# Kernel tuning notes

Hardware: AMD Instinct MI355X
Metric: run time of the kernel (lower is better)

The kernel has to match this reference:

```python
import jax, jax.numpy as jnp
import numpy as np
import itertools


def _dwconv(x, w, b, pad, dil):
    # depthwise conv3d, x: [B,C,H,W,D], w: [C,1,k,k,k]
    out = jax.lax.conv_general_dilated(
        x, w, (1, 1, 1), [(pad, pad)] * 3, rhs_dilation=(dil, dil, dil),
        dimension_numbers=('NCDHW', 'OIDHW', 'NCDHW'), feature_group_count=x.shape[1])
    return out + b[None, :, None, None, None]


def _conv(x, w, b, pad):
    out = jax.lax.conv_general_dilated(
        x, w, (1, 1, 1), [(pad, pad)] * 3,
        dimension_numbers=('NCDHW', 'OIDHW', 'NCDHW'))
    return out + b[None, :, None, None, None]


def _pw(x, w, b):
    # 1x1x1 conv: x [B,C,H,W,D], w [O,C]
    return jnp.einsum('bchwd,oc->bohwd', x, w) + b[None, :, None, None, None]


def _deform_conv3d(x, off_w, off_b, w, b):
    # DeformConvPack-style: offsets from a regular 3x3x3 conv, then
    # trilinearly-interpolated gather at (base + kernel tap + offset), then GEMM.
    B, C, H, W, D = x.shape
    K = 27
    dt = x.dtype
    off = _conv(x, off_w, off_b, 1).reshape(B, K, 3, H, W, D)  # per-tap (dh,dw,dd)
    gh = jnp.arange(H, dtype=dt)
    gw = jnp.arange(W, dtype=dt)
    gd = jnp.arange(D, dtype=dt)
    base = jnp.stack(jnp.meshgrid(gh, gw, gd, indexing='ij'), 0)  # [3,H,W,D]
    t = jnp.arange(-1, 2, dtype=dt)  # kernel taps, padding=1
    taps = jnp.stack(jnp.meshgrid(t, t, t, indexing='ij'), -1).reshape(K, 3)
    pos = base[None] + taps[:, :, None, None, None]  # [K,3,H,W,D]
    pos = pos[None] + off  # [B,K,3,H,W,D]
    i0 = jnp.floor(pos)
    frac = pos - i0  # [B,K,3,H,W,D]
    i0 = i0.astype(jnp.int32)
    N = H * W * D
    xf = x.reshape(B, C, N)
    hi = jnp.array([H - 1, W - 1, D - 1], jnp.int32)[None, None, :, None, None, None]
    acc = jnp.zeros((B, C, K * N), dt)
    for corner in itertools.product((0, 1), repeat=3):
        c = jnp.array(corner, jnp.int32)[None, None, :, None, None, None]
        idx = i0 + c
        wgt = jnp.prod(jnp.where(c == 1, frac, 1.0 - frac), axis=2)  # [B,K,H,W,D]
        valid = jnp.all((idx >= 0) & (idx <= hi), axis=2)
        ic = jnp.clip(idx, 0, hi)
        flat = (ic[:, :, 0] * W + ic[:, :, 1]) * D + ic[:, :, 2]  # [B,K,H,W,D]
        g = jnp.take_along_axis(xf, flat.reshape(B, 1, K * N), axis=2)  # [B,C,K*N]
        acc = acc + g * (wgt * valid.astype(dt)).reshape(B, 1, K * N)
    sampled = acc.reshape(B, C, K, N)
    out = jnp.einsum('bckn,ock->bon', sampled, w.reshape(w.shape[0], C, K))
    out = out + b[None, :, None]
    return out.reshape(B, -1, H, W, D)


def _forward(x, proj1_w, proj1_b, conv0_w, conv0_b, convsp_w, convsp_b,
             off_w, off_b, dcn_w, dcn_b, conv1_w, conv1_b, proj2_w, proj2_b,
             B, C, H, W, D):
    xv = jnp.transpose(x, (0, 2, 1)).reshape(B, C, H, W, D)
    shortcut = xv
    h = jax.nn.gelu(_pw(xv, proj1_w, proj1_b), approximate=False)
    u = h
    a = _dwconv(h, conv0_w, conv0_b, 2, 1)        # 5x5x5 depthwise
    a = _dwconv(a, convsp_w, convsp_b, 9, 3)      # 7x7x7 depthwise, dilation 3
    a = _deform_conv3d(a, off_w, off_b, dcn_w, dcn_b)
    a = _pw(a, conv1_w, conv1_b)
    h = u * a
    h = _pw(h, proj2_w, proj2_b)
    out = h + shortcut
    return jnp.transpose(out.reshape(B, C, H * W * D), (0, 2, 1))


def setup_inputs() -> dict:
    key = jax.random.key(0)
    ks = jax.random.split(key, 8)
    B, C, H, W, D = 1, 64, 32, 32, 32
    N = H * W * D
    r = lambda k, s, sc: jax.random.normal(k, s, jnp.float32) * np.float32(sc)
    inv = lambda f: 1.0 / np.sqrt(f)
    return {
        'x': jax.random.normal(ks[0], (B, N, C), jnp.float32),
        'proj1_w': r(ks[1], (C, C), inv(C)), 'proj1_b': jnp.zeros((C,), jnp.float32),
        'conv0_w': r(ks[2], (C, 1, 5, 5, 5), inv(125)), 'conv0_b': jnp.zeros((C,), jnp.float32),
        'convsp_w': r(ks[3], (C, 1, 7, 7, 7), inv(343)), 'convsp_b': jnp.zeros((C,), jnp.float32),
        'off_w': r(ks[4], (81, C, 3, 3, 3), 0.01 * inv(27 * C)), 'off_b': jnp.zeros((81,), jnp.float32),
        'dcn_w': r(ks[5], (C, C, 3, 3, 3), inv(27 * C)), 'dcn_b': jnp.zeros((C,), jnp.float32),
        'conv1_w': r(ks[6], (C, C), inv(C)), 'conv1_b': jnp.zeros((C,), jnp.float32),
        'proj2_w': r(ks[7], (C, C), inv(C)), 'proj2_b': jnp.zeros((C,), jnp.float32),
        'B': B, 'C': C, 'H': H, 'W': W, 'D': D,
    }


def reference(x, proj1_w, proj1_b, conv0_w, conv0_b, convsp_w, convsp_b,
              off_w, off_b, dcn_w, dcn_b, conv1_w, conv1_b, proj2_w, proj2_b,
              B, C, H, W, D):
    return _forward(x, proj1_w, proj1_b, conv0_w, conv0_b, convsp_w, convsp_b,
                    off_w, off_b, dcn_w, dcn_b, conv1_w, conv1_b, proj2_w, proj2_b,
                    B, C, H, W, D)
```

## Files before the change

kernel.cpp:

```cpp
#include <hip/hip_runtime.h>
#include <math.h>

#define NSP 32768
#define NCH 64

typedef _Float16 half8 __attribute__((ext_vector_type(8)));
typedef _Float16 half4 __attribute__((ext_vector_type(4)));
typedef _Float16 half2v __attribute__((ext_vector_type(2)));
typedef float f32x4 __attribute__((ext_vector_type(4)));

__global__ __launch_bounds__(256) void k_proj1m(const float* __restrict__ x,
        const half8* __restrict__ Wp1, const float* __restrict__ b,
        _Float16* __restrict__ Uh) {
    __shared__ __align__(16) _Float16 Sx[64 * 72];
    int t = threadIdx.x;
    int n0 = blockIdx.x * 64;
    int lane = t & 63, wv = t >> 6;
    for (int i = wv; i < 64; i += 4) {
        float v = x[(size_t)(n0 + i) * 64 + lane];
        Sx[i * 72 + lane] = (_Float16)v;
    }
    __syncthreads();
    int pl = lane & 15, g = lane >> 4;
    int ob = wv;
    const half8* wbase = Wp1 + ob * 64 + lane;
    #pragma unroll
    for (int nt = 0; nt < 4; ++nt) {
        f32x4 acc4 = {0.f, 0.f, 0.f, 0.f};
        const _Float16* sb = &Sx[(nt * 16 + pl) * 72 + g * 8];
        #pragma unroll
        for (int kb = 0; kb < 2; ++kb) {
            half8 af = wbase[kb * 256];
            half8 bf = *(const half8*)(sb + kb * 32);
            acc4 = __builtin_amdgcn_mfma_f32_16x16x32_f16(af, bf, acc4, 0, 0, 0);
        }
        int n = n0 + nt * 16 + pl;
        #pragma unroll
        for (int r = 0; r < 4; ++r) {
            int o = ob * 16 + g * 4 + r;
            float a = acc4[r] + b[o];
            float gv = 0.5f * a * (1.0f + erff(a * 0.70710678118654752f));
            Uh[(size_t)o * NSP + n] = (_Float16)gv;
        }
    }
}

__global__ __launch_bounds__(256) void k_dw5(const _Float16* __restrict__ in,
        const float* __restrict__ w, const float* __restrict__ b,
        _Float16* __restrict__ out) {
    __shared__ float Sb5[2][20 * 38];
    int t = threadIdx.x;
    int bid = blockIdx.x;
    int blk = (bid & 7) * 128 + (bid >> 3);
    int c  = blk >> 4;
    int hq = (blk >> 1) & 7;
    int wq = blk & 1;
    int d  = t & 31;
    int wbloc = t >> 5;
    int wb = wq * 8 + wbloc;
    const float* wc = w + c * 125;
    const _Float16* src = in + ((size_t)c << 15);

    for (int idx = t; idx < 160; idx += 256) {
        int bi = idx / 80, r = idx % 80;
        int wi = r >> 2, e = r & 3;
        int Dp = (e < 2) ? e : 32 + e;
        Sb5[bi][wi * 38 + Dp] = 0.f;
    }

    float bc = b[c];
    float acc[4][2];
    #pragma unroll
    for (int a = 0; a < 4; ++a) { acc[a][0] = bc; acc[a][1] = bc; }

    #define STAGE5(m)                                                        \
        { int hh_ = 4 * hq + (m) - 2;                                        \
          if ((unsigned)hh_ < 32u) {                                         \
            const _Float16* row_ = src + (hh_ << 10);                        \
            for (int idx = t; idx < 80; idx += 256) {                        \
                int wi = idx >> 2, oct = idx & 3;                            \
                int wj = 16 * wq - 2 + wi;                                   \
                half8 vv = (half8)(_Float16)0.f;                             \
                if ((unsigned)wj < 32u)                                      \
                    vv = *(const half8*)&row_[(wj << 5) + oct * 8];          \
                float* dst = &Sb5[(m) & 1][wi * 38 + 2 + oct * 8];           \
                dst[0] = (float)vv[0]; dst[1] = (float)vv[1];                \
                dst[2] = (float)vv[2]; dst[3] = (float)vv[3];                \
                dst[4] = (float)vv[4]; dst[5] = (float)vv[5];                \
                dst[6] = (float)vv[6]; dst[7] = (float)vv[7];                \
            } } }

    STAGE5(0)
    __syncthreads();
    #pragma unroll 1
    for (int m = 0; m < 8; ++m) {
        if (m < 7) STAGE5(m + 1)
        int hh = 4 * hq + m - 2;
        if ((unsigned)hh < 32u) {
            float v[6][5];
            const float* sb = &Sb5[m & 1][0];
            #pragma unroll
            for (int jc = 0; jc < 6; ++jc)
                #pragma unroll
                for (int l = 0; l < 5; ++l)
                    v[jc][l] = sb[(2 * wbloc + jc) * 38 + d + l];
            #pragma unroll
            for (int a = 0; a < 4; ++a) {
                if (a <= m && m <= a + 4) {
                    const float* wr = wc + (m - a) * 25;
                    float s0 = 0.f, s1 = 0.f;
                    #pragma unroll
                    for (int j = 0; j < 5; ++j)
                        #pragma unroll
                        for (int l = 0; l < 5; ++l) {
                            float wv2 = wr[j * 5 + l];
                            s0 += wv2 * v[j][l];
                            s1 += wv2 * v[j + 1][l];
                        }
                    acc[a][0] += s0;
                    acc[a][1] += s1;
                }
            }
        }
        __syncthreads();
    }
    #pragma unroll
    for (int a = 0; a < 4; ++a)
        #pragma unroll
        for (int bb = 0; bb < 2; ++bb)
            out[(size_t)c * NSP + ((4 * hq + a) << 10) + ((2 * wb + bb) << 5) + d]
                = (_Float16)acc[a][bb];
    #undef STAGE5
}

__global__ __launch_bounds__(256) void k_dw7(const _Float16* __restrict__ in,
        const float* __restrict__ w, const float* __restrict__ b,
        _Float16* __restrict__ out) {
    __shared__ float Sb7[2][26 * 52];
    int t = threadIdx.x;
    int bid = blockIdx.x;
    int blk = (bid & 7) * 96 + (bid >> 3);
    int c  = blk / 12;
    int h0 = (blk % 12) >> 2;
    int wq = blk & 3;
    int d  = t & 31;
    int wloc = t >> 5;
    int w_ = wq * 8 + wloc;
    const float* wc = w + c * 343;
    const _Float16* src = in + ((size_t)c << 15);

    for (int idx = t; idx < 936; idx += 256) {
        int bi = idx / 468, r = idx % 468;
        int wi = r / 18, e = r % 18;
        int Dp = (e < 9) ? e : 32 + e;
        Sb7[bi][wi * 52 + Dp] = 0.f;
    }

    float bc = b[c];
    float acc[11];
    #pragma unroll
    for (int a = 0; a < 11; ++a) acc[a] = bc;

    #define STAGE7(m)                                                        \
        { int hh_ = h0 + 3 * (m) - 9;                                        \
          if ((unsigned)hh_ < 32u) {                                         \
            const _Float16* row_ = src + (hh_ << 10);                        \
            for (int idx = t; idx < 104; idx += 256) {                       \
                int wi = idx >> 2, oct = idx & 3;                            \
                int wj = 8 * wq - 9 + wi;                                    \
                half8 vv = (half8)(_Float16)0.f;                             \
                if ((unsigned)wj < 32u)                                      \
                    vv = *(const half8*)&row_[(wj << 5) + oct * 8];          \
                float* dst = &Sb7[(m) & 1][wi * 52 + 9 + oct * 8];           \
                dst[0] = (float)vv[0]; dst[1] = (float)vv[1];                \
                dst[2] = (float)vv[2]; dst[3] = (float)vv[3];                \
                dst[4] = (float)vv[4]; dst[5] = (float)vv[5];                \
                dst[6] = (float)vv[6]; dst[7] = (float)vv[7];                \
            } } }

    STAGE7(0)
    __syncthreads();
    #pragma unroll 1
    for (int m = 0; m < 17; ++m) {
        if (m < 16) STAGE7(m + 1)
        int hh = h0 + 3 * m - 9;
        if ((unsigned)hh < 32u) {
            float vf[49];
            const float* sb = &Sb7[m & 1][0];
            #pragma unroll
            for (int jw = 0; jw < 7; ++jw)
                #pragma unroll
                for (int l = 0; l < 7; ++l)
                    vf[jw * 7 + l] = sb[(wloc + 3 * jw) * 52 + d + 3 * l];
            #pragma unroll
            for (int a = 0; a < 11; ++a) {
                if (a <= m && m <= a + 6) {
                    const float* wr = wc + (m - a) * 49;
                    float sA = 0.f, sB = 0.f;
                    #pragma unroll
                    for (int q = 0; q < 24; ++q) {
                        sA = fmaf(wr[2 * q],     vf[2 * q],     sA);
                        sB = fmaf(wr[2 * q + 1], vf[2 * q + 1], sB);
                    }
                    acc[a] += sA + sB + wr[48] * vf[48];
                }
            }
        }
        __syncthreads();
    }
    #pragma unroll
    for (int a = 0; a < 11; ++a) {
        int h = h0 + 3 * a;
        if (h < 32)
            out[(size_t)c * NSP + (h << 10) + (w_ << 5) + d] = (_Float16)acc[a];
    }
    #undef STAGE7
}

__global__ __launch_bounds__(256) void k_tr(const _Float16* __restrict__ in,
        _Float16* __restrict__ outh) {
    __shared__ __align__(16) _Float16 tile[64 * 74];
    int t = threadIdx.x;
    int n0 = blockIdx.x * 64;
    #pragma unroll
    for (int i = 0; i < 2; ++i) {
        int u = i * 256 + t;
        int c = u >> 3, oct = u & 7;
        half8 v = *(const half8*)&in[(size_t)c * NSP + n0 + oct * 8];
        *(half8*)&tile[c * 74 + oct * 8] = v;
    }
    __syncthreads();
    #pragma unroll
    for (int i = 0; i < 2; ++i) {
        int u = i * 256 + t;
        int nl = u >> 3, co = u & 7;
        half8 r;
        #pragma unroll
        for (int j = 0; j < 8; ++j) r[j] = tile[(co * 8 + j) * 74 + nl];
        *(half8*)&outh[(size_t)(n0 + nl) * 64 + co * 8] = r;
    }
}

__global__ __launch_bounds__(256) void k_wpack_all(
        const float* __restrict__ p1w, const float* __restrict__ c1w,
        const float* __restrict__ p2w, const float* __restrict__ dcw,
        const float* __restrict__ ofw,
        _Float16* __restrict__ Wp1, _Float16* __restrict__ Wc1,
        _Float16* __restrict__ Wp2f, _Float16* __restrict__ Wp,
        _Float16* __restrict__ Wp2) {
    int bidx = blockIdx.x;
    int t = threadIdx.x;
    if (bidx < 48) {
        const float* w = (bidx < 16) ? p1w : (bidx < 32) ? c1w : p2w;
        _Float16* Wd   = (bidx < 16) ? Wp1 : (bidx < 32) ? Wc1 : Wp2f;
        int idx = (bidx & 15) * 256 + t;
        int j = idx & 7;
        int l = (idx >> 3) & 63;
        int obk = idx >> 9;
        int ob = obk & 3, kb = obk >> 2;
        int o = ob * 16 + (l & 15);
        int Kp = kb * 32 + (l >> 4) * 8 + j;
        Wd[idx] = (_Float16)w[o * 64 + Kp];
    } else if (bidx < 480) {
        int idx = (bidx - 48) * 256 + t;
        int j = idx & 7;
        int l = (idx >> 3) & 63;
        int obk = idx >> 9;
        int ob = obk & 3, kb = obk >> 2;
        int o = ob * 16 + (l & 15);
        int Kp = kb * 32 + (l >> 4) * 8 + j;
        int k = Kp >> 6, c = Kp & 63;
        Wp[idx] = (_Float16)dcw[(size_t)o * 1728 + c * 27 + k];
    } else {
        int idx = (bidx - 480) * 256 + t;
        int j = idx & 7;
        int l = (idx >> 3) & 63;
        int obk = idx >> 9;
        int ob = obk % 6, kb = obk / 6;
        int o = ob * 16 + (l & 15);
        int Kp = kb * 32 + (l >> 4) * 8 + j;
        int k = Kp >> 6, c = Kp & 63;
        Wp2[idx] = (o < 81) ? (_Float16)ofw[(size_t)o * 1728 + c * 27 + k]
                            : (_Float16)0.f;
    }
}

__global__ __launch_bounds__(384) void k_offg(const _Float16* __restrict__ aTh,
        const half8* __restrict__ Wp2, const float* __restrict__ obias,
        _Float16* __restrict__ OFFn) {
    __shared__ __align__(16) char SMEM[29376];
    _Float16* S2  = (_Float16*)SMEM;
    _Float16* TFh = (_Float16*)SMEM;
    const int SB = 3 * 34 * 72;
    int t = threadIdx.x;
    int bid = blockIdx.x;
    int blk = (bid & 7) * 128 + (bid >> 3);
    int h = blk >> 5, w = blk & 31;
    int n0 = blk << 5;
    int lane = t & 63, wv = t >> 6;
    int co8 = (lane & 7) << 3;

    for (int u = t; u < 864; u += 384) {
        int bi = u / 432, r2 = u % 432;
        int nbw = r2 / 144, r3 = r2 % 144;
        int dd = (r3 >= 72) ? 33 : 0, cc = r3 % 72;
        S2[bi * SB + (nbw * 34 + dd) * 72 + cc] = (_Float16)0.f;
    }

    int pl = lane & 15, g = lane >> 4;
    int obi = wv;
    f32x4 acc[2];
    acc[0] = (f32x4){0.f, 0.f, 0.f, 0.f};
    acc[1] = (f32x4){0.f, 0.f, 0.f, 0.f};
    const half8* wb = Wp2 + obi * 64 + lane;

    #define OSTAGE(kh)                                                        \
        { int hh_ = h + (kh) - 1;                                            \
          bool okh_ = (unsigned)hh_ < 32u;                                   \
          for (int u = wv; u < 12; u += 6) {                                 \
              int nbw = u >> 2, oct = u & 3;                                 \
              int wj = w + nbw - 1;                                          \
              int di = oct * 8 + (lane >> 3);                                \
              bool ok = okh_ & ((unsigned)wj < 32u);                         \
              half8 vv = (half8)(_Float16)0.f;                               \
              if (ok) vv = *(const half8*)(aTh +                             \
                  ((size_t)((((hh_ << 5) + wj) << 5) + di)) * 64 + co8);     \
              *(half8*)&S2[((kh) & 1) * SB + (nbw * 34 + 1 + di) * 72 + co8] \
                  = vv;                                                      \
          } }

    #define OCOMP(kh)                                                        \
        { const _Float16* sb = &S2[((kh) & 1) * SB + pl * 72 + g * 8];       \
          _Pragma("unroll")                                                  \
          for (int kk = 0; kk < 18; ++kk) {                                  \
              int kglob = (kh) * 9 + (kk >> 1);                              \
              int kw3 = (kglob / 3) % 3, kd = kglob % 3;                     \
              half8 af = wb[(size_t)((kh) * 18 + kk) * 384];                 \
              _Pragma("unroll")                                              \
              for (int pt = 0; pt < 2; ++pt) {                               \
                  int row = kw3 * 34 + pt * 16 + kd;                         \
                  half8 bf = *(const half8*)(sb + row * 72 + (kk & 1) * 32); \
                  acc[pt] = __builtin_amdgcn_mfma_f32_16x16x32_f16(          \
                                af, bf, acc[pt], 0, 0, 0);                   \
              }                                                              \
          } }

    OSTAGE(0)
    __syncthreads();
    OSTAGE(1)
    OCOMP(0)
    __syncthreads();
    OSTAGE(2)
    OCOMP(1)
    __syncthreads();
    OCOMP(2)
    #undef OSTAGE
    #undef OCOMP

    __syncthreads();
    #pragma unroll
    for (int pt = 0; pt < 2; ++pt) {
        int pos = pt * 16 + pl;
        #pragma unroll
        for (int r = 0; r < 4; ++r) {
            int o = obi * 16 + g * 4 + r;
            if (o < 81) {
                int slot = (o / 3) * 4 + o % 3;
                TFh[pos * 108 + slot] = (_Float16)(acc[pt][r] + obias[o]);
            }
        }
    }
    __syncthreads();
    for (int u = t; u < 864; u += 384) {
        int row = u / 27, q = u - row * 27;
        half4 v = *(const half4*)&TFh[row * 108 + q * 4];
        *(half4*)&OFFn[(size_t)(n0 + row) * 108 + q * 4] = v;
    }
}

__global__ __launch_bounds__(256) void k_deform(const _Float16* __restrict__ aTh,
        const _Float16* __restrict__ OFFn, const half8* __restrict__ Wp,
        const float* __restrict__ db, _Float16* __restrict__ dcnT) {
    __shared__ __align__(16) _Float16 S[32 * 328];
    __shared__ __align__(16) _Float16 TPF[864 * 4];
    __shared__ int TPv[864];
    int t = threadIdx.x;
    int bid = blockIdx.x;
    int blk = (bid & 7) * 128 + (bid >> 3);
    int n0 = blk * 32;
    int lane = t & 63, wv = t >> 6;

    for (int idx = t; idx < 864; idx += 256) {
        int p = idx & 31, k = idx >> 5;
        int n = n0 + p;
        int h = n >> 10, w = (n >> 5) & 31, d = n & 31;
        half4 ov4 = *(const half4*)&OFFn[(size_t)n * 108 + k * 4];
        float ph = (float)(h + k / 9 - 1)       + (float)ov4[0];
        float pw = (float)(w + (k / 3) % 3 - 1) + (float)ov4[1];
        float pd = (float)(d + k % 3 - 1)       + (float)ov4[2];
        float fh = floorf(ph), fw = floorf(pw), fd = floorf(pd);
        int ih = (int)fh, iw = (int)fw, id = (int)fd;
        int nb0 = ih * 1024 + iw * 32 + id;
        int mask = 0;
        #pragma unroll
        for (int cb = 0; cb < 8; ++cb) {
            int hh = ih + ((cb >> 2) & 1);
            int wq = iw + ((cb >> 1) & 1);
            int dq = id + (cb & 1);
            bool ok = ((unsigned)hh < 32u) & ((unsigned)wq < 32u) & ((unsigned)dq < 32u);
            mask |= (ok ? 1 : 0) << cb;
        }
        TPv[idx] = ((nb0 + 4096) << 8) | mask;
        half4 f;
        f[0] = (_Float16)(ph - fh);
        f[1] = (_Float16)(pw - fw);
        f[2] = (_Float16)(pd - fd);
        f[3] = (_Float16)0.f;
        *(half4*)&TPF[idx * 4] = f;
    }
    __syncthreads();

    int p8 = lane >> 3, co = lane & 7;
    int pl = lane & 15, g = lane >> 4;
    f32x4 acc[2];
    acc[0] = (f32x4){0.f, 0.f, 0.f, 0.f};
    acc[1] = (f32x4){0.f, 0.f, 0.f, 0.f};
    const half8* wbase = Wp + wv * 64 + lane;
    const _Float16* sbase0 = &S[pl * 328 + g * 8];
    const _Float16* sbase1 = &S[(16 + pl) * 328 + g * 8];

    #define DCHUNK(T0, NT)                                                   \
        for (int u = wv; u < (NT) * 4; u += 4) {                             \
            int kk = u >> 2, pg = u & 3;                                     \
            int p = pg * 8 + p8;                                             \
            int tap = ((T0) + kk) * 32 + p;                                  \
            int v = TPv[tap];                                                \
            int nb = (v >> 8) - 4096, mask = v & 255;                        \
            int snb = nb < 0 ? 0 : (nb > 32767 ? 32767 : nb);                \
            half4 f = *(const half4*)&TPF[tap * 4];                          \
            _Float16 one = (_Float16)1.f;                                    \
            _Float16 rh = f[0], rw = f[1], rd = f[2];                        \
            _Float16 h0 = one - rh, w0 = one - rw, d0 = one - rd;            \
            _Float16 t00 = h0 * w0, t01 = h0 * rw;                           \
            _Float16 t10 = rh * w0, t11 = rh * rw;                           \
            half2v a0 = (half2v)0, a1 = (half2v)0, a2 = (half2v)0,           \
                   a3 = (half2v)0;                                           \
            _Pragma("unroll")                                                \
            for (int i = 0; i < 8; ++i) {                                    \
                int nn = nb + ((i >> 2) & 1) * 1024 + ((i >> 1) & 1) * 32    \
                       + (i & 1);                                            \
                bool okc = (mask >> i) & 1;                                  \
                size_t ad = (size_t)(okc ? nn : snb) << 6;                   \
                half8 vv = *(const half8*)(aTh + ad + (co << 3));            \
                _Float16 txy = (i & 4) ? ((i & 2) ? t11 : t10)               \
                                       : ((i & 2) ? t01 : t00);              \
                _Float16 wg = txy * ((i & 1) ? rd : d0);                     \
                wg = okc ? wg : (_Float16)0.f;                               \
                half2v wg2 = {wg, wg};                                       \
                a0 += (half2v){vv[0], vv[1]} * wg2;                          \
                a1 += (half2v){vv[2], vv[3]} * wg2;                          \
                a2 += (half2v){vv[4], vv[5]} * wg2;                          \
                a3 += (half2v){vv[6], vv[7]} * wg2;                          \
            }                                                                \
            half8 r;                                                         \
            r[0] = a0[0]; r[1] = a0[1]; r[2] = a1[0]; r[3] = a1[1];          \
            r[4] = a2[0]; r[5] = a2[1]; r[6] = a3[0]; r[7] = a3[1];          \
            *(half8*)&S[p * 328 + kk * 64 + (co << 3)] = r;                  \
        }                                                                    \
        __syncthreads();                                                     \
        _Pragma("unroll")                                                    \
        for (int kb = 0; kb < (NT) * 2; ++kb) {                              \
            half8 af = wbase[(size_t)(2 * (T0) + kb) * 256];                 \
            half8 bf0 = *(const half8*)(sbase0 + kb * 32);                   \
            half8 bf1 = *(const half8*)(sbase1 + kb * 32);                   \
            acc[0] = __builtin_amdgcn_mfma_f32_16x16x32_f16(af, bf0,         \
                         acc[0], 0, 0, 0);                                   \
            acc[1] = __builtin_amdgcn_mfma_f32_16x16x32_f16(af, bf1,         \
                         acc[1], 0, 0, 0);                                   \
        }                                                                    \
        __syncthreads();

    DCHUNK(0, 5)
    DCHUNK(5, 5)
    DCHUNK(10, 5)
    DCHUNK(15, 5)
    DCHUNK(20, 5)
    DCHUNK(25, 2)
    #undef DCHUNK

    #pragma unroll
    for (int pt = 0; pt < 2; ++pt) {
        half4 hv;
        #pragma unroll
        for (int r2 = 0; r2 < 4; ++r2) {
            int o = wv * 16 + g * 4 + r2;
            hv[r2] = (_Float16)(acc[pt][r2] + db[o]);
        }
        *(half4*)&dcnT[(size_t)(n0 + pt * 16 + pl) * 64 + wv * 16 + g * 4] = hv;
    }
}

__global__ __launch_bounds__(256) void k_finalm(const _Float16* __restrict__ dcnT,
        const _Float16* __restrict__ Uh, const float* __restrict__ x,
        const half8* __restrict__ Wc1, const float* __restrict__ c1b,
        const half8* __restrict__ Wp2f, const float* __restrict__ p2b,
        float* __restrict__ out) {
    __shared__ __align__(16) _Float16 Sd[64 * 72];
    __shared__ __align__(16) _Float16 Sh[64 * 72];
    int t = threadIdx.x;
    int n0 = blockIdx.x * 64;
    int lane = t & 63, wv = t >> 6;
    #pragma unroll
    for (int i = 0; i < 2; ++i) {
        int u = i * 256 + t;
        int nl = u >> 3, oct = u & 7;
        *(half8*)&Sd[nl * 72 + oct * 8] =
            *(const half8*)&dcnT[(size_t)(n0 + nl) * 64 + oct * 8];
    }
    __syncthreads();

    int pl = lane & 15, g = lane >> 4;
    int ob = wv;
    const half8* w1 = Wc1 + ob * 64 + lane;
    #pragma unroll
    for (int nt = 0; nt < 4; ++nt) {
        f32x4 acc4 = {0.f, 0.f, 0.f, 0.f};
        const _Float16* sb = &Sd[(nt * 16 + pl) * 72 + g * 8];
        #pragma unroll
        for (int kb = 0; kb < 2; ++kb) {
            half8 af = w1[kb * 256];
            half8 bf = *(const half8*)(sb + kb * 32);
            acc4 = __builtin_amdgcn_mfma_f32_16x16x32_f16(af, bf, acc4, 0, 0, 0);
        }
        int n = n0 + nt * 16 + pl;
        int o0 = ob * 16 + g * 4;
        float4 bb = *(const float4*)&c1b[o0];
        half4 hv;
        hv[0] = (_Float16)((float)Uh[(size_t)(o0 + 0) * NSP + n] * (acc4[0] + bb.x));
        hv[1] = (_Float16)((float)Uh[(size_t)(o0 + 1) * NSP + n] * (acc4[1] + bb.y));
        hv[2] = (_Float16)((float)Uh[(size_t)(o0 + 2) * NSP + n] * (acc4[2] + bb.z));
        hv[3] = (_Float16)((float)Uh[(size_t)(o0 + 3) * NSP + n] * (acc4[3] + bb.w));
        *(half4*)&Sh[(nt * 16 + pl) * 72 + o0] = hv;
    }
    __syncthreads();

    const half8* w2 = Wp2f + ob * 64 + lane;
    #pragma unroll
    for (int nt = 0; nt < 4; ++nt) {
        f32x4 acc4 = {0.f, 0.f, 0.f, 0.f};
        const _Float16* sb = &Sh[(nt * 16 + pl) * 72 + g * 8];
        #pragma unroll
        for (int kb = 0; kb < 2; ++kb) {
            half8 af = w2[kb * 256];
            half8 bf = *(const half8*)(sb + kb * 32);
            acc4 = __builtin_amdgcn_mfma_f32_16x16x32_f16(af, bf, acc4, 0, 0, 0);
        }
        int n = n0 + nt * 16 + pl;
        int o0 = ob * 16 + g * 4;
        float4 bb = *(const float4*)&p2b[o0];
        float4 xr = *(const float4*)&x[(size_t)n * 64 + o0];
        float4 ov;
        ov.x = acc4[0] + bb.x + xr.x;
        ov.y = acc4[1] + bb.y + xr.y;
        ov.z = acc4[2] + bb.z + xr.z;
        ov.w = acc4[3] + bb.w + xr.w;
        *(float4*)&out[(size_t)n * 64 + o0] = ov;
    }
}

extern "C" void kernel_launch(void* const* d_in, const int* in_sizes, int n_in,
                              void* d_out, int out_size, void* d_ws, size_t ws_size,
                              hipStream_t stream) {
    const float* x   = (const float*)d_in[0];
    const float* p1w = (const float*)d_in[1];
    const float* p1b = (const float*)d_in[2];
    const float* c0w = (const float*)d_in[3];
    const float* c0b = (const float*)d_in[4];
    const float* csw = (const float*)d_in[5];
    const float* csb = (const float*)d_in[6];
    const float* ofw = (const float*)d_in[7];
    const float* ofb = (const float*)d_in[8];
    const float* dcw = (const float*)d_in[9];
    const float* dcb = (const float*)d_in[10];
    const float* c1w = (const float*)d_in[11];
    const float* c1b = (const float*)d_in[12];
    const float* p2w = (const float*)d_in[13];
    const float* p2b = (const float*)d_in[14];
    float* out = (float*)d_out;

    char* ws = (char*)d_ws;
    const size_t CN2 = (size_t)NCH * NSP * 2;
    _Float16* Uh   = (_Float16*)(ws);
    _Float16* T0h  = (_Float16*)(ws + CN2);
    _Float16* T1h  = (_Float16*)(ws + 2 * CN2);
    _Float16* aTh  = (_Float16*)(ws + 3 * CN2);
    _Float16* OFFn = (_Float16*)(ws + 4 * CN2);
    _Float16* dcnT = (_Float16*)(ws + 4 * CN2 + (size_t)NSP * 108 * 2);
    _Float16* Wp   = dcnT + (size_t)NSP * 64;
    _Float16* Wp2  = Wp + 110592;
    _Float16* Wp1  = Wp2 + 165888;
    _Float16* Wc1  = Wp1 + 4096;
    _Float16* Wp2f = Wc1 + 4096;

    k_wpack_all<<<1128, 256, 0, stream>>>(p1w, c1w, p2w, dcw, ofw,
                                          Wp1, Wc1, Wp2f, Wp, Wp2);
    k_proj1m   <<<NSP / 64, 256, 0, stream>>>(x, (const half8*)Wp1, p1b, Uh);
    k_dw5      <<<1024, 256, 0, stream>>>(Uh, c0w, c0b, T0h);
    k_dw7      <<<768, 256, 0, stream>>>(T0h, csw, csb, T1h);
    k_tr       <<<NSP / 64, 256, 0, stream>>>(T1h, aTh);
    k_offg     <<<1024, 384, 0, stream>>>(aTh, (const half8*)Wp2, ofb, OFFn);
    k_deform   <<<1024, 256, 0, stream>>>(aTh, OFFn, (const half8*)Wp, dcb, dcnT);
    k_finalm   <<<NSP / 64, 256, 0, stream>>>(dcnT, Uh, x, (const half8*)Wc1, c1b,
                                              (const half8*)Wp2f, p2b, out);
}
```

Measured before the change: 120.1 us.

## Stage per-tap 3x3 halo of activations in LDS for deform gather

The deformable-conv gather now stages a halo of the input activations into shared memory for each (kh,kw) tap pair and 32-channel half. Samples whose offsets stay within one voxel of the nominal tap read from LDS, and samples that land farther away fall back to global memory. The loop is restructured into 18 chunks, each loading the next chunk's halo while the current chunk's MFMAs run, which shrinks the S buffer. The cost is more barriers, extra redundant global loads to fill the halo, a larger LDS footprint that may reduce occupancy, and divergent branches.

```diff
diff --git a/kernel.cpp b/kernel.cpp
--- a/kernel.cpp
+++ b/kernel.cpp
@@ -381,26 +381,34 @@
 __global__ __launch_bounds__(256) void k_deform(const _Float16* __restrict__ aTh,
         const _Float16* __restrict__ OFFn, const half8* __restrict__ Wp,
         const float* __restrict__ db, _Float16* __restrict__ dcnT) {
-    __shared__ __align__(16) _Float16 S[32 * 328];
+    __shared__ __align__(16) _Float16 HALO[9 * 36 * 36];
+    __shared__ __align__(16) _Float16 S[32 * 104];
     __shared__ __align__(16) _Float16 TPF[864 * 4];
     __shared__ int TPv[864];
     int t = threadIdx.x;
     int bid = blockIdx.x;
     int blk = (bid & 7) * 128 + (bid >> 3);
     int n0 = blk * 32;
+    int h = blk >> 5, w = blk & 31;
     int lane = t & 63, wv = t >> 6;
 
     for (int idx = t; idx < 864; idx += 256) {
         int p = idx & 31, k = idx >> 5;
         int n = n0 + p;
-        int h = n >> 10, w = (n >> 5) & 31, d = n & 31;
+        int kh = k / 9 - 1, kw = (k / 3) % 3 - 1, kd = k % 3 - 1;
         half4 ov4 = *(const half4*)&OFFn[(size_t)n * 108 + k * 4];
-        float ph = (float)(h + k / 9 - 1)       + (float)ov4[0];
-        float pw = (float)(w + (k / 3) % 3 - 1) + (float)ov4[1];
-        float pd = (float)(d + k % 3 - 1)       + (float)ov4[2];
+        float ph = (float)(h + kh) + (float)ov4[0];
+        float pw = (float)(w + kw) + (float)ov4[1];
+        float pd = (float)(p + kd) + (float)ov4[2];
         float fh = floorf(ph), fw = floorf(pw), fd = floorf(pd);
         int ih = (int)fh, iw = (int)fw, id = (int)fd;
         int nb0 = ih * 1024 + iw * 32 + id;
+        int rh0 = ih - h - kh + 1;
+        int rw0 = iw - w - kw + 1;
+        int rd0 = id - p - kd + 1;
+        bool far = ((unsigned)rh0 > 1u) | ((unsigned)rw0 > 1u)
+                 | ((unsigned)rd0 > 1u);
+        int lf = far ? 255 : ((rh0 << 7) | (rw0 << 6) | (id + 2));
         int mask = 0;
         #pragma unroll
         for (int cb = 0; cb < 8; ++cb) {
@@ -415,78 +423,131 @@
         f[0] = (_Float16)(ph - fh);
         f[1] = (_Float16)(pw - fw);
         f[2] = (_Float16)(pd - fd);
-        f[3] = (_Float16)0.f;
+        f[3] = (_Float16)(float)lf;
         *(half4*)&TPF[idx * 4] = f;
     }
     __syncthreads();
 
-    int p8 = lane >> 3, co = lane & 7;
+    int p16 = lane >> 2, co = lane & 3;
     int pl = lane & 15, g = lane >> 4;
     f32x4 acc[2];
     acc[0] = (f32x4){0.f, 0.f, 0.f, 0.f};
     acc[1] = (f32x4){0.f, 0.f, 0.f, 0.f};
     const half8* wbase = Wp + wv * 64 + lane;
-    const _Float16* sbase0 = &S[pl * 328 + g * 8];
-    const _Float16* sbase1 = &S[(16 + pl) * 328 + g * 8];
-
-    #define DCHUNK(T0, NT)                                                   \
-        for (int u = wv; u < (NT) * 4; u += 4) {                             \
-            int kk = u >> 2, pg = u & 3;                                     \
-            int p = pg * 8 + p8;                                             \
-            int tap = ((T0) + kk) * 32 + p;                                  \
-            int v = TPv[tap];                                                \
-            int nb = (v >> 8) - 4096, mask = v & 255;                        \
-            int snb = nb < 0 ? 0 : (nb > 32767 ? 32767 : nb);                \
-            half4 f = *(const half4*)&TPF[tap * 4];                          \
-            _Float16 one = (_Float16)1.f;                                    \
-            _Float16 rh = f[0], rw = f[1], rd = f[2];                        \
-            _Float16 h0 = one - rh, w0 = one - rw, d0 = one - rd;            \
-            _Float16 t00 = h0 * w0, t01 = h0 * rw;                           \
-            _Float16 t10 = rh * w0, t11 = rh * rw;                           \
-            half2v a0 = (half2v)0, a1 = (half2v)0, a2 = (half2v)0,           \
-                   a3 = (half2v)0;                                           \
-            _Pragma("unroll")                                                \
-            for (int i = 0; i < 8; ++i) {                                    \
-                int nn = nb + ((i >> 2) & 1) * 1024 + ((i >> 1) & 1) * 32    \
-                       + (i & 1);                                            \
-                bool okc = (mask >> i) & 1;                                  \
-                size_t ad = (size_t)(okc ? nn : snb) << 6;                   \
-                half8 vv = *(const half8*)(aTh + ad + (co << 3));            \
-                _Float16 txy = (i & 4) ? ((i & 2) ? t11 : t10)               \
-                                       : ((i & 2) ? t01 : t00);              \
-                _Float16 wg = txy * ((i & 1) ? rd : d0);                     \
-                wg = okc ? wg : (_Float16)0.f;                               \
-                half2v wg2 = {wg, wg};                                       \
-                a0 += (half2v){vv[0], vv[1]} * wg2;                          \
-                a1 += (half2v){vv[2], vv[3]} * wg2;                          \
-                a2 += (half2v){vv[4], vv[5]} * wg2;                          \
-                a3 += (half2v){vv[6], vv[7]} * wg2;                          \
-            }                                                                \
-            half8 r;                                                         \
-            r[0] = a0[0]; r[1] = a0[1]; r[2] = a1[0]; r[3] = a1[1];          \
-            r[4] = a2[0]; r[5] = a2[1]; r[6] = a3[0]; r[7] = a3[1];          \
-            *(half8*)&S[p * 328 + kk * 64 + (co << 3)] = r;                  \
-        }                                                                    \
-        __syncthreads();                                                     \
-        _Pragma("unroll")                                                    \
-        for (int kb = 0; kb < (NT) * 2; ++kb) {                              \
-            half8 af = wbase[(size_t)(2 * (T0) + kb) * 256];                 \
-            half8 bf0 = *(const half8*)(sbase0 + kb * 32);                   \
-            half8 bf1 = *(const half8*)(sbase1 + kb * 32);                   \
-            acc[0] = __builtin_amdgcn_mfma_f32_16x16x32_f16(af, bf0,         \
-                         acc[0], 0, 0, 0);                                   \
-            acc[1] = __builtin_amdgcn_mfma_f32_16x16x32_f16(af, bf1,         \
-                         acc[1], 0, 0, 0);                                   \
-        }                                                                    \
+    const _Float16* sbase0 = &S[pl * 104 + g * 8];
+    const _Float16* sbase1 = &S[(16 + pl) * 104 + g * 8];
+
+    #define DSTAGE(cc)                                                       \
+        { int khkw_ = (cc) >> 1, cb_ = (cc) & 1;                             \
+          int kh_ = khkw_ / 3 - 1, kw_ = khkw_ % 3 - 1;                      \
+          int bh_ = h + kh_ - 1, bw_ = w + kw_ - 1;                          \
+          for (int i = t; i < 1296; i += 256) {                              \
+              int r_ = i / 144;                                              \
+              int rem_ = i - r_ * 144;                                       \
+              int dd_ = rem_ >> 2, c4_ = rem_ & 3;                           \
+              int hh_ = bh_ + r_ / 3;                                        \
+              int ww_ = bw_ + r_ % 3;                                        \
+              int dq_ = dd_ - 2;                                             \
+              bool ok_ = ((unsigned)hh_ < 32u) & ((unsigned)ww_ < 32u)       \
+                       & ((unsigned)dq_ < 32u);                              \
+              half8 vv_ = (half8)(_Float16)0.f;                              \
+              if (ok_) vv_ = *(const half8*)&aTh[                            \
+                  (size_t)(((hh_ << 5) + ww_) * 32 + dq_) * 64               \
+                  + cb_ * 32 + c4_ * 8];                                     \
+              *(half8*)&HALO[(r_ * 36 + dd_) * 36 + c4_ * 8] = vv_;          \
+          } }
+
+    #define DGATHER(cc)                                                      \
+        { int khkw_ = (cc) >> 1, cb_ = (cc) & 1;                             \
+          for (int u = wv; u < 6; u += 4) {                                  \
+              int kd_ = u >> 1, pgh_ = u & 1;                                \
+              int p_ = pgh_ * 16 + p16;                                      \
+              int tap = (khkw_ * 3 + kd_) * 32 + p_;                         \
+              int v_ = TPv[tap];                                             \
+              int nb_ = (v_ >> 8) - 4096, mask_ = v_ & 255;                  \
+              half4 f_ = *(const half4*)&TPF[tap * 4];                      \
+              int lf_ = (int)(float)f_[3];                                   \
+              _Float16 one_ = (_Float16)1.f;                                 \
+              _Float16 rh_ = f_[0], rw_ = f_[1], rd_ = f_[2];                \
+              _Float16 h0_ = one_ - rh_, w0_ = one_ - rw_, d0_ = one_ - rd_; \
+              _Float16 t00_ = h0_ * w0_, t01_ = h0_ * rw_;                   \
+              _Float16 t10_ = rh_ * w0_, t11_ = rh_ * rw_;                   \
+              half2v a0_ = (half2v)0, a1_ = (half2v)0, a2_ = (half2v)0,      \
+                     a3_ = (half2v)0;                                        \
+              if (lf_ != 255) {                                              \
+                  int rh0_ = (lf_ >> 7) & 1, rw0_ = (lf_ >> 6) & 1;          \
+                  int idl_ = lf_ & 63;                                       \
+                  _Pragma("unroll")                                          \
+                  for (int i = 0; i < 8; ++i) {                              \
+                      int r_ = (rh0_ + ((i >> 2) & 1)) * 3                   \
+                             + (rw0_ + ((i >> 1) & 1));                      \
+                      int dd_ = idl_ + (i & 1);                              \
+                      half8 vv_ = *(const half8*)&HALO[                      \
+                          (r_ * 36 + dd_) * 36 + co * 8];                    \
+                      _Float16 txy_ = (i & 4) ? ((i & 2) ? t11_ : t10_)      \
+                                             : ((i & 2) ? t01_ : t00_);      \
+                      _Float16 wg_ = txy_ * ((i & 1) ? rd_ : d0_);           \
+                      half2v wg2_ = {wg_, wg_};                              \
+                      a0_ += (half2v){vv_[0], vv_[1]} * wg2_;                \
+                      a1_ += (half2v){vv_[2], vv_[3]} * wg2_;                \
+                      a2_ += (half2v){vv_[4], vv_[5]} * wg2_;                \
+                      a3_ += (half2v){vv_[6], vv_[7]} * wg2_;                \
+                  }                                                          \
+              } else {                                                       \
+                  int snb_ = nb_ < 0 ? 0 : (nb_ > 32767 ? 32767 : nb_);      \
+                  _Pragma("unroll")                                          \
+                  for (int i = 0; i < 8; ++i) {                              \
+                      int nn_ = nb_ + ((i >> 2) & 1) * 1024                  \
+                              + ((i >> 1) & 1) * 32 + (i & 1);               \
+                      bool okc_ = (mask_ >> i) & 1;                          \
+                      size_t ad_ = (size_t)(okc_ ? nn_ : snb_) << 6;         \
+                      half8 vv_ = *(const half8*)(aTh + ad_ + cb_ * 32       \
+                                                  + co * 8);                 \
+                      _Float16 txy_ = (i & 4) ? ((i & 2) ? t11_ : t10_)      \
+                                             : ((i & 2) ? t01_ : t00_);      \
+                      _Float16 wg_ = txy_ * ((i & 1) ? rd_ : d0_);           \
+                      wg_ = okc_ ? wg_ : (_Float16)0.f;                      \
+                      half2v wg2_ = {wg_, wg_};                              \
+                      a0_ += (half2v){vv_[0], vv_[1]} * wg2_;                \
+                      a1_ += (half2v){vv_[2], vv_[3]} * wg2_;                \
+                      a2_ += (half2v){vv_[4], vv_[5]} * wg2_;                \
+                      a3_ += (half2v){vv_[6], vv_[7]} * wg2_;                \
+                  }                                                          \
+              }                                                              \
+              half8 r8_;                                                     \
+              r8_[0] = a0_[0]; r8_[1] = a0_[1]; r8_[2] = a1_[0];             \
+              r8_[3] = a1_[1]; r8_[4] = a2_[0]; r8_[5] = a2_[1];             \
+              r8_[6] = a3_[0]; r8_[7] = a3_[1];                              \
+              *(half8*)&S[p_ * 104 + kd_ * 32 + co * 8] = r8_;               \
+          } }
+
+    #define DMFMA(cc)                                                        \
+        { int khkw_ = (cc) >> 1, cb_ = (cc) & 1;                             \
+          _Pragma("unroll")                                                  \
+          for (int kd_ = 0; kd_ < 3; ++kd_) {                                \
+              int kbg_ = (khkw_ * 3 + kd_) * 2 + cb_;                        \
+              half8 af_ = wbase[(size_t)kbg_ * 256];                         \
+              half8 bf0_ = *(const half8*)(sbase0 + kd_ * 32);               \
+              half8 bf1_ = *(const half8*)(sbase1 + kd_ * 32);               \
+              acc[0] = __builtin_amdgcn_mfma_f32_16x16x32_f16(af_, bf0_,     \
+                           acc[0], 0, 0, 0);                                 \
+              acc[1] = __builtin_amdgcn_mfma_f32_16x16x32_f16(af_, bf1_,     \
+                           acc[1], 0, 0, 0);                                 \
+          } }
+
+    DSTAGE(0)
+    __syncthreads();
+    #pragma unroll 1
+    for (int cc = 0; cc < 18; ++cc) {
+        DGATHER(cc)
         __syncthreads();
-
-    DCHUNK(0, 5)
-    DCHUNK(5, 5)
-    DCHUNK(10, 5)
-    DCHUNK(15, 5)
-    DCHUNK(20, 5)
-    DCHUNK(25, 2)
-    #undef DCHUNK
+        if (cc < 17) DSTAGE(cc + 1)
+        DMFMA(cc)
+        __syncthreads();
+    }
+    #undef DSTAGE
+    #undef DGATHER
+    #undef DMFMA
 
     #pragma unroll
     for (int pt = 0; pt < 2; ++pt) {
```

After: 145.3 us. +21.0%, slower.
